# Kernel optimization log

Hardware: AMD Instinct MI355X
Metric: run time of the kernel (lower is better)

Reference implementation:

```python
import jax, jax.numpy as jnp
import numpy as np
from functools import partial

RES = 512          # image resolution (source uses 1024; scaled for CPU baseline)
BLOB_COUNT = 2048  # number of Gaussian blobs (source uses 4096)
CHUNK = 64         # blobs processed per scan step to bound intermediates


def setup_inputs() -> dict:
    key = jax.random.key(0)
    k_pos, k_scale, k_rot, k_col = jax.random.split(key, 4)
    pos = jax.random.uniform(k_pos, (BLOB_COUNT, 2))                      # blob centers in [0,1]^2
    scale = 0.005 + 0.05 * jax.random.uniform(k_scale, (BLOB_COUNT, 2))   # per-axis std dev
    rot = 2.0 * jnp.pi * jax.random.uniform(k_rot, (BLOB_COUNT, 1))       # rotation angle
    color = jax.random.uniform(k_col, (BLOB_COUNT, 3))                    # rgb intensity
    blobs = jnp.concatenate([pos, scale, rot, color], axis=-1).astype(jnp.float32)  # [N, 8]
    return {"blobs": blobs}


def _splat(blobs):
    H = W = RES
    # pixel centers in normalized [0,1] coords
    ys = (jnp.arange(H, dtype=jnp.float32) + 0.5) / H
    xs = (jnp.arange(W, dtype=jnp.float32) + 0.5) / W
    py, px = jnp.meshgrid(ys, xs, indexing="ij")  # [H, W]

    def body(img, chunk):  # chunk: [CHUNK, 8]
        pos = chunk[:, 0:2]
        sx = chunk[:, 2][:, None, None]
        sy = chunk[:, 3][:, None, None]
        rot = chunk[:, 4]
        color = chunk[:, 5:8]
        c = jnp.cos(rot)[:, None, None]
        s = jnp.sin(rot)[:, None, None]
        dx = px[None] - pos[:, 0][:, None, None]   # [C, H, W]
        dy = py[None] - pos[:, 1][:, None, None]
        xr = c * dx + s * dy                        # rotate into blob frame
        yr = -s * dx + c * dy
        g = jnp.exp(-0.5 * ((xr / sx) ** 2 + (yr / sy) ** 2))  # [C, H, W]
        img = img + jnp.einsum("chw,ck->hwk", g, color)
        return img, None

    img0 = jnp.zeros((H, W, 3), dtype=blobs.dtype)
    chunks = blobs.reshape(BLOB_COUNT // CHUNK, CHUNK, 8)
    img, _ = jax.lax.scan(jax.checkpoint(body), img0, chunks)
    return img


@jax.jit
def reference(blobs):
    return _splat(blobs)
```

## Files before the change

kernel.cpp:

```cpp
#include <hip/hip_runtime.h>
#include <math.h>

#define RES     512
#define NBLOB   2048
#define TILE_W  32
#define TILE_H  8
#define TX_N    (RES / TILE_W)
#define TY_N    (RES / TILE_H)
#define PRE_STRIDE 16
#define CHUNK_B 256
#define NCHUNK  (NBLOB / CHUNK_B)
#define CULL_R5 4.9956f

__device__ __forceinline__ float fast_exp2(float x) {
#if __has_builtin(__builtin_amdgcn_exp2f)
    return __builtin_amdgcn_exp2f(x);
#else
    return exp2f(x);
#endif
}

__global__ __launch_bounds__(256) void pre_kernel(const float* __restrict__ blobs,
                                                  float* __restrict__ pre) {
    int i = blockIdx.x * blockDim.x + threadIdx.x;
    if (i >= NBLOB) return;
    const float* bp = blobs + i * 8;
    float posx = bp[0], posy = bp[1];
    float sx = bp[2], sy = bp[3];
    float rot = bp[4];
    float c = cosf(rot), s = sinf(rot);
    const float K = 0.84932184f;
    float isx = K / sx, isy = K / sy;
    float* o = pre + i * PRE_STRIDE;
    o[0] = posx;
    o[1] = posy;
    o[2] = c * isx;
    o[3] = s * isx;
    o[4] = -s * isy;
    o[5] = c * isy;
    o[6] = bp[5];
    o[7] = bp[6];
    o[8] = bp[7];
    o[9] = 0.f; o[10] = 0.f; o[11] = 0.f;

    float hx = CULL_R5 * sqrtf(c * c * sx * sx + s * s * sy * sy);
    float hy = CULL_R5 * sqrtf(s * s * sx * sx + c * c * sy * sy);
    int tx0 = max(0,        (int)floorf(((posx - hx) * RES - 0.5f) * (1.0f / TILE_W)));
    int tx1 = min(TX_N - 1, (int)floorf(((posx + hx) * RES - 0.5f) * (1.0f / TILE_W)));
    int ty0 = max(0,        (int)floorf(((posy - hy) * RES - 0.5f) * (1.0f / TILE_H)));
    int ty1 = min(TY_N - 1, (int)floorf(((posy + hy) * RES - 0.5f) * (1.0f / TILE_H)));
    int* ob = (int*)(o + 12);
    ob[0] = tx0; ob[1] = tx1; ob[2] = ty0; ob[3] = ty1;
}

__global__ __launch_bounds__(256) void splat_kernel(const float* __restrict__ pre,
                                                    float* __restrict__ out) {
    __shared__ int sh_cnt[NCHUNK];
    __shared__ float4 sh_p0[CHUNK_B];
    __shared__ float4 sh_p1[CHUNK_B];
    __shared__ float  sh_p2[CHUNK_B];

    const int tid = threadIdx.x;
    const int lane = tid & 63;
    const int tx = blockIdx.x;
    const int ty = blockIdx.y;

    if (tid < NCHUNK) sh_cnt[tid] = 0;

    const int x = tx * TILE_W + (tid & 31);
    const int y = ty * TILE_H + (tid >> 5);
    const float fx = (x + 0.5f) * (1.0f / RES);
    const float fy = (y + 0.5f) * (1.0f / RES);

    float ar = 0.f, ag = 0.f, ab = 0.f;

    __syncthreads();

    for (int c = 0; c < NCHUNK; ++c) {
        const int j = c * CHUNK_B + tid;
        const int4 ob = *(const int4*)(pre + j * PRE_STRIDE + 12);
        const bool hit = (tx >= ob.x) & (tx <= ob.y) & (ty >= ob.z) & (ty <= ob.w);
        const unsigned long long mask = __ballot(hit);
        const int total = __popcll(mask);
        int base = 0;
        if (lane == 0 && total > 0) base = atomicAdd(&sh_cnt[c], total);
        base = __builtin_amdgcn_readfirstlane(base);
        if (hit) {
            const int pos = base + __popcll(mask & ((1ull << lane) - 1ull));
            const float4* p4 = (const float4*)(pre + j * PRE_STRIDE);
            sh_p0[pos] = p4[0];
            sh_p1[pos] = p4[1];
            sh_p2[pos] = p4[2].x;
        }
        __syncthreads();

        const int n = sh_cnt[c];
        #pragma unroll 4
        for (int k = 0; k < n; ++k) {
            const float4 p0 = sh_p0[k];
            const float4 p1 = sh_p1[k];
            const float  cb = sh_p2[k];
            const float dx = fx - p0.x;
            const float dy = fy - p0.y;
            const float u = p0.z * dx + p0.w * dy;
            const float v = p1.x * dx + p1.y * dy;
            const float g = fast_exp2(-(u * u + v * v));
            ar += g * p1.z;
            ag += g * p1.w;
            ab += g * cb;
        }
        __syncthreads();
    }

    const int base = (y * RES + x) * 3;
    out[base + 0] = ar;
    out[base + 1] = ag;
    out[base + 2] = ab;
}

extern "C" void kernel_launch(void* const* d_in, const int* in_sizes, int n_in,
                              void* d_out, int out_size, void* d_ws, size_t ws_size,
                              hipStream_t stream) {
    const float* blobs = (const float*)d_in[0];
    float* out = (float*)d_out;
    float* pre = (float*)d_ws;

    hipLaunchKernelGGL(pre_kernel, dim3(NBLOB / 256), dim3(256), 0, stream,
                       blobs, pre);
    hipLaunchKernelGGL(splat_kernel, dim3(TX_N, TY_N), dim3(256), 0, stream,
                       pre, out);
}
```

Baseline: 85.81 us.

## Compute two pixel rows per thread with taller tiles to amortize blob loads

Doubles tile height to 16 rows while keeping 256 threads, so each thread accumulates two pixels eight rows apart. The second pixel's rotated coordinates come from the first by adding a constant offset, and the shared-memory blob parameters are loaded once for both pixels. This halves the number of blocks and the culling/compaction passes, and cuts LDS traffic per pixel. In exchange, taller tiles pull in more blobs per tile, so more work is spent on Gaussians that contribute nothing, and each thread uses more registers.

```diff
diff --git a/kernel.cpp b/kernel.cpp
--- a/kernel.cpp
+++ b/kernel.cpp
@@ -4,7 +4,8 @@
 #define RES     512
 #define NBLOB   2048
 #define TILE_W  32
-#define TILE_H  8
+#define TILE_H  16
+#define ROWS_T  8
 #define TX_N    (RES / TILE_W)
 #define TY_N    (RES / TILE_H)
 #define PRE_STRIDE 16
@@ -67,12 +68,14 @@
 
     if (tid < NCHUNK) sh_cnt[tid] = 0;
 
-    const int x = tx * TILE_W + (tid & 31);
-    const int y = ty * TILE_H + (tid >> 5);
-    const float fx = (x + 0.5f) * (1.0f / RES);
-    const float fy = (y + 0.5f) * (1.0f / RES);
+    const int x  = tx * TILE_W + (tid & 31);
+    const int y0 = ty * TILE_H + (tid >> 5);
+    const float fx  = (x + 0.5f) * (1.0f / RES);
+    const float fy0 = (y0 + 0.5f) * (1.0f / RES);
+    const float DY  = (float)ROWS_T * (1.0f / RES);
 
-    float ar = 0.f, ag = 0.f, ab = 0.f;
+    float ar0 = 0.f, ag0 = 0.f, ab0 = 0.f;
+    float ar1 = 0.f, ag1 = 0.f, ab1 = 0.f;
 
     __syncthreads();
 
@@ -101,21 +104,31 @@
             const float4 p1 = sh_p1[k];
             const float  cb = sh_p2[k];
             const float dx = fx - p0.x;
-            const float dy = fy - p0.y;
-            const float u = p0.z * dx + p0.w * dy;
-            const float v = p1.x * dx + p1.y * dy;
-            const float g = fast_exp2(-(u * u + v * v));
-            ar += g * p1.z;
-            ag += g * p1.w;
-            ab += g * cb;
+            const float dy = fy0 - p0.y;
+            const float u0 = p0.z * dx + p0.w * dy;
+            const float v0 = p1.x * dx + p1.y * dy;
+            const float u1 = u0 + p0.w * DY;
+            const float v1 = v0 + p1.y * DY;
+            const float g0 = fast_exp2(-(u0 * u0 + v0 * v0));
+            const float g1 = fast_exp2(-(u1 * u1 + v1 * v1));
+            ar0 += g0 * p1.z;
+            ag0 += g0 * p1.w;
+            ab0 += g0 * cb;
+            ar1 += g1 * p1.z;
+            ag1 += g1 * p1.w;
+            ab1 += g1 * cb;
         }
         __syncthreads();
     }
 
-    const int base = (y * RES + x) * 3;
-    out[base + 0] = ar;
-    out[base + 1] = ag;
-    out[base + 2] = ab;
+    const int b0 = (y0 * RES + x) * 3;
+    out[b0 + 0] = ar0;
+    out[b0 + 1] = ag0;
+    out[b0 + 2] = ab0;
+    const int b1 = ((y0 + ROWS_T) * RES + x) * 3;
+    out[b1 + 0] = ar1;
+    out[b1 + 1] = ag1;
+    out[b1 + 2] = ab1;
 }
 
 extern "C" void kernel_launch(void* const* d_in, const int* in_sizes, int n_in,
```

Measured after the change: 85.32 us. Within noise of the previous version (-0.6%).
